# Kernel tuning notes

Hardware: AMD Instinct MI355X
Metric: run time of the kernel (lower is better)

The kernel has to match this reference:

```python
import jax, jax.numpy as jnp
import numpy as np

N = 50000      # nodes
E = 600000     # edges
C = 128        # input/output channels
H = 128        # hidden channels
EA = 8         # edge_attr_dim


def _lin_init(key, fan_in, fan_out):
    kw, kb = jax.random.split(key)
    w = jax.random.normal(kw, (fan_in, fan_out), dtype=jnp.float32) / np.sqrt(fan_in)
    b = jax.random.normal(kb, (fan_out,), dtype=jnp.float32) * 0.01
    return w, b


def setup_inputs() -> dict:
    key = jax.random.key(0)
    ks = jax.random.split(key, 8)
    x = jax.random.normal(ks[0], (N, C), dtype=jnp.float32)
    coord = jax.random.normal(ks[1], (N, 3), dtype=jnp.float32)
    edge_index = jax.random.randint(ks[2], (2, E), 0, N, dtype=jnp.int64)
    edge_attr = jax.random.normal(ks[3], (E, EA), dtype=jnp.float32)
    # edge_mlp: Linear(2C+1+EA -> H), ReLU, Linear(H -> H), ReLU
    w_e1, b_e1 = _lin_init(ks[4], 2 * C + 1 + EA, H)
    w_e2, b_e2 = _lin_init(ks[5], H, H)
    # node_mlp: Linear(H + C -> H), ReLU, Linear(H -> C)
    w_n1, b_n1 = _lin_init(ks[6], H + C, H)
    w_n2, b_n2 = _lin_init(ks[7], H, C)
    return {"x": x, "coord": coord, "edge_index": edge_index, "edge_attr": edge_attr,
            "w_e1": w_e1, "b_e1": b_e1, "w_e2": w_e2, "b_e2": b_e2,
            "w_n1": w_n1, "b_n1": b_n1, "w_n2": w_n2, "b_n2": b_n2}


def reference(x, coord, edge_index, edge_attr,
              w_e1, b_e1, w_e2, b_e2, w_n1, b_n1, w_n2, b_n2):
    row, col = edge_index[0], edge_index[1]
    # coord2radial: per-edge squared distance (coord_diff normalization unused
    # downstream since equivariant=False -> coord branch not taken)
    coord_diff = coord[row] - coord[col]                 # [E, 3]
    radial = jnp.sum(coord_diff * coord_diff, axis=1, keepdims=True)  # [E, 1]
    # edge_model: concat(source, target, radial, edge_attr) -> MLP
    e_in = jnp.concatenate([x[row], x[col], radial, edge_attr], axis=1)  # [E, 2C+1+EA]
    h = jax.nn.relu(e_in @ w_e1 + b_e1)
    edge_feat = jax.nn.relu(h @ w_e2 + b_e2)             # [E, H]
    # node_model: unsorted_segment_sum over row, concat with x, node MLP
    agg = jax.ops.segment_sum(edge_feat, row, num_segments=x.shape[0])  # [N, H]
    n_in = jnp.concatenate([x, agg], axis=1)             # [N, C+H]
    out = jax.nn.relu(n_in @ w_n1 + b_n1) @ w_n2 + b_n2  # [N, C]
    return out
```

## Files before the change

kernel.cpp:

```cpp
#include <hip/hip_runtime.h>

#define CH  128
#define HID 128
#define EAD 8

__device__ __forceinline__ void load8(const float* __restrict__ p, float* r) {
    float4 v0 = *(const float4*)p;
    float4 v1 = *(const float4*)(p + 4);
    r[0]=v0.x; r[1]=v0.y; r[2]=v0.z; r[3]=v0.w;
    r[4]=v1.x; r[5]=v1.y; r[6]=v1.z; r[7]=v1.w;
}
__device__ __forceinline__ void store8(float* p, const float* v) {
    *(float4*)p       = make_float4(v[0], v[1], v[2], v[3]);
    *(float4*)(p + 4) = make_float4(v[4], v[5], v[6], v[7]);
}
__device__ __forceinline__ void zero88(float a[8][8]) {
#pragma unroll
    for (int i = 0; i < 8; i++)
#pragma unroll
        for (int j = 0; j < 8; j++) a[i][j] = 0.f;
}

template <int K>
__device__ __forceinline__ void gemm_tile8(const float* sA, int strideA,
                                           const float* __restrict__ B, int ldb,
                                           int tr8, int jb, float acc[8][8]) {
#pragma unroll 2
    for (int k = 0; k < K; k += 4) {
        float av[8][4];
#pragma unroll
        for (int i = 0; i < 8; i++) {
            float4 t = *(const float4*)(sA + (tr8 + 8 * i) * strideA + k);
            av[i][0] = t.x; av[i][1] = t.y; av[i][2] = t.z; av[i][3] = t.w;
        }
#pragma unroll
        for (int kk = 0; kk < 4; kk++) {
            float b8[8];
            load8(B + (size_t)(k + kk) * ldb + jb, b8);
#pragma unroll
            for (int i = 0; i < 8; i++)
#pragma unroll
                for (int j = 0; j < 8; j++)
                    acc[i][j] = fmaf(av[i][kk], b8[j], acc[i][j]);
        }
    }
}

__global__ __launch_bounds__(128, 2)
void precompute_kernel(const float* __restrict__ x, const float* __restrict__ w1,
                       const float* __restrict__ b1, float* __restrict__ tbl, int N) {
    __shared__ float sX[64 * 132];
    const int tid = threadIdx.x;
    const int n0  = blockIdx.x * 64;
    {
        const int n = tid >> 1, q = tid & 1;
        int gn = n0 + n; if (gn >= N) gn = N - 1;
        const float4* src = (const float4*)(x + (size_t)gn * CH + q * 64);
        float4* dst = (float4*)(sX + n * 132 + q * 64);
#pragma unroll
        for (int u = 0; u < 16; u++) dst[u] = src[u];
    }
    __syncthreads();
    const int tr8 = tid & 7, jb = (tid >> 3) * 8;
    float acc[8][8];

    zero88(acc);
    gemm_tile8<128>(sX, 132, w1, HID, tr8, jb, acc);
    float bb[8]; load8(b1 + jb, bb);
#pragma unroll
    for (int i = 0; i < 8; i++) {
        const int gn = n0 + tr8 + 8 * i;
        if (gn < N) {
            float v[8];
#pragma unroll
            for (int j = 0; j < 8; j++) v[j] = acc[i][j] + bb[j];
            store8(tbl + (size_t)gn * 256 + jb, v);
        }
    }

    zero88(acc);
    gemm_tile8<128>(sX, 132, w1 + CH * HID, HID, tr8, jb, acc);
#pragma unroll
    for (int i = 0; i < 8; i++) {
        const int gn = n0 + tr8 + 8 * i;
        if (gn < N) store8(tbl + (size_t)gn * 256 + 128 + jb, acc[i]);
    }
}

__global__ void hist_kernel(const int* __restrict__ ei, int* __restrict__ deg, int E) {
    const int e = blockIdx.x * blockDim.x + threadIdx.x;
    if (e < E) atomicAdd(&deg[ei[e]], 1);
}

__global__ void scan_kernel(const int* __restrict__ deg, int* __restrict__ row_ptr,
                            int* __restrict__ cursor, int N) {
    __shared__ int part[1024];
    const int tid = threadIdx.x;
    const int chunk = (N + 1023) / 1024;
    const int lo = tid * chunk;
    const int hi = (lo + chunk < N) ? lo + chunk : N;
    int s = 0;
    for (int i = lo; i < hi; i++) s += deg[i];
    part[tid] = s;
    __syncthreads();
    for (int off = 1; off < 1024; off <<= 1) {
        int v = (tid >= off) ? part[tid - off] : 0;
        __syncthreads();
        part[tid] += v;
        __syncthreads();
    }
    int run = (tid == 0) ? 0 : part[tid - 1];
    for (int i = lo; i < hi; i++) {
        row_ptr[i] = run; cursor[i] = run;
        run += deg[i];
    }
    if (tid == 1023) row_ptr[N] = run;
}

__global__ void scatter_kernel(const int* __restrict__ ei, int* cursor,
                               int* __restrict__ perm, int E) {
    const int e = blockIdx.x * blockDim.x + threadIdx.x;
    if (e < E) {
        const int p = atomicAdd(&cursor[ei[e]], 1);
        perm[p] = e;
    }
}

__global__ __launch_bounds__(128, 2)
void edge_kernel_sorted(const float* __restrict__ tbl, const float* __restrict__ coord,
                        const int* __restrict__ ei, const float* __restrict__ ea,
                        const float* __restrict__ w1, const float* __restrict__ w2,
                        const float* __restrict__ b2, const int* __restrict__ perm,
                        const int* __restrict__ row_ptr, float* agg, int E) {
    __shared__ float sH[64 * 132];
    __shared__ float sW[9 * 128];
    __shared__ int   sRow[64];
    const int tid = threadIdx.x;

    const int nwg = gridDim.x;
    const int qq = nwg >> 3, rr = nwg & 7;
    const int xcd = blockIdx.x & 7, idx = blockIdx.x >> 3;
    const int wg  = (xcd < rr) ? (xcd * (qq + 1) + idx)
                               : (rr * (qq + 1) + (xcd - rr) * qq + idx);
    const int e0  = wg * 64;

    for (int i = tid; i < 9 * 128; i += 128) sW[i] = w1[256 * HID + i];
    __syncthreads();

    {
        const int s = tid >> 1, q = tid & 1;
        const int pe = perm[e0 + s];
        const int r = ei[pe];
        const int c = ei[E + pe];
        if (q == 0) sRow[s] = r;
        const float dx = coord[3 * r + 0] - coord[3 * c + 0];
        const float dy = coord[3 * r + 1] - coord[3 * c + 1];
        const float dz = coord[3 * r + 2] - coord[3 * c + 2];
        const float radial = fmaf(dx, dx, fmaf(dy, dy, dz * dz));
        float eav[8];
        load8(ea + (size_t)pe * EAD, eav);
        const float* tr = tbl + (size_t)r * 256 + q * 64;
        const float* tc = tbl + (size_t)c * 256 + 128 + q * 64;
        float* dst = sH + s * 132 + q * 64;
#pragma unroll
        for (int u = 0; u < 8; u++) {
            float hr[8], hc[8], wr[8], v[8];
            load8(tr + u * 8, hr);
            load8(tc + u * 8, hc);
            load8(sW + q * 64 + u * 8, wr);
#pragma unroll
            for (int j = 0; j < 8; j++) v[j] = hr[j] + hc[j] + radial * wr[j];
#pragma unroll
            for (int m = 0; m < 8; m++) {
                float we[8];
                load8(sW + (1 + m) * 128 + q * 64 + u * 8, we);
#pragma unroll
                for (int j = 0; j < 8; j++) v[j] = fmaf(eav[m], we[j], v[j]);
            }
#pragma unroll
            for (int j = 0; j < 8; j++) v[j] = fmaxf(v[j], 0.f);
            store8(dst + u * 8, v);
        }
    }
    __syncthreads();

    const int tr8 = tid & 7, jb = (tid >> 3) * 8;
    float acc[8][8];
    zero88(acc);
    gemm_tile8<128>(sH, 132, w2, HID, tr8, jb, acc);
    float bb[8]; load8(b2 + jb, bb);
    __syncthreads();

#pragma unroll
    for (int i = 0; i < 8; i++) {
        float v[8];
#pragma unroll
        for (int j = 0; j < 8; j++) v[j] = fmaxf(acc[i][j] + bb[j], 0.f);
        store8(sH + (tr8 + 8 * i) * 132 + jb, v);
    }
    __syncthreads();

#pragma unroll
    for (int base = 0; base < 64; base += 32) {
        const int s = base + (tid >> 2), q4 = tid & 3;
        const int r = sRow[s];
        const bool head = (s == 0) || (sRow[s - 1] != r);
        if (head) {
            float sum[32];
            const float* src = sH + s * 132 + q4 * 32;
#pragma unroll
            for (int j = 0; j < 32; j += 4) {
                float4 t = *(const float4*)(src + j);
                sum[j] = t.x; sum[j+1] = t.y; sum[j+2] = t.z; sum[j+3] = t.w;
            }
            int L = 1;
            while (s + L < 64 && sRow[s + L] == r) {
                const float* p = sH + (s + L) * 132 + q4 * 32;
#pragma unroll
                for (int j = 0; j < 32; j += 4) {
                    float4 t = *(const float4*)(p + j);
                    sum[j] += t.x; sum[j+1] += t.y; sum[j+2] += t.z; sum[j+3] += t.w;
                }
                L++;
            }
            float* dst = agg + (size_t)r * HID + q4 * 32;
            const bool interior = (row_ptr[r] >= e0) && (row_ptr[r + 1] <= e0 + 64);
            if (interior) {
#pragma unroll
                for (int j = 0; j < 32; j += 4)
                    *(float4*)(dst + j) = make_float4(sum[j], sum[j+1], sum[j+2], sum[j+3]);
            } else {
#pragma unroll
                for (int j = 0; j < 32; j++) atomicAdd(dst + j, sum[j]);
            }
        }
    }
}

__global__ __launch_bounds__(128, 2)
void node_kernel(const float* __restrict__ x, const float* agg,
                 const float* __restrict__ w1, const float* __restrict__ b1,
                 const float* __restrict__ w2, const float* __restrict__ b2,
                 float* out, int N) {
    __shared__ float sA[64 * 260];
    const int tid = threadIdx.x;
    const int n0  = blockIdx.x * 64;
    {
        const int n = tid >> 1, q = tid & 1;
        int gn = n0 + n; if (gn >= N) gn = N - 1;
        const float4* src = q ? (const float4*)(agg + (size_t)gn * HID)
                              : (const float4*)(x   + (size_t)gn * CH);
        float4* dst = (float4*)(sA + n * 260 + q * CH);
#pragma unroll
        for (int u = 0; u < 32; u++) dst[u] = src[u];
    }
    __syncthreads();
    const int tr8 = tid & 7, jb = (tid >> 3) * 8;
    float acc[8][8];
    zero88(acc);
    gemm_tile8<256>(sA, 260, w1, HID, tr8, jb, acc);
    float bb[8]; load8(b1 + jb, bb);
    float h[8][8];
#pragma unroll
    for (int i = 0; i < 8; i++)
#pragma unroll
        for (int j = 0; j < 8; j++) h[i][j] = fmaxf(acc[i][j] + bb[j], 0.f);
    __syncthreads();
#pragma unroll
    for (int i = 0; i < 8; i++) store8(sA + (tr8 + 8 * i) * 260 + jb, h[i]);
    __syncthreads();
    zero88(acc);
    gemm_tile8<128>(sA, 260, w2, CH, tr8, jb, acc);
    float b2v[8]; load8(b2 + jb, b2v);
#pragma unroll
    for (int i = 0; i < 8; i++) {
        const int gn = n0 + tr8 + 8 * i;
        if (gn < N) {
            float v[8];
#pragma unroll
            for (int j = 0; j < 8; j++) v[j] = acc[i][j] + b2v[j];
            store8(out + (size_t)gn * CH + jb, v);
        }
    }
}

extern "C" void kernel_launch(void* const* d_in, const int* in_sizes, int n_in,
                              void* d_out, int out_size, void* d_ws, size_t ws_size,
                              hipStream_t stream) {
    const float* x     = (const float*)d_in[0];
    const float* coord = (const float*)d_in[1];
    const int*   ei    = (const int*)d_in[2];
    const float* ea    = (const float*)d_in[3];
    const float* w_e1  = (const float*)d_in[4];
    const float* b_e1  = (const float*)d_in[5];
    const float* w_e2  = (const float*)d_in[6];
    const float* b_e2  = (const float*)d_in[7];
    const float* w_n1  = (const float*)d_in[8];
    const float* b_n1  = (const float*)d_in[9];
    const float* w_n2  = (const float*)d_in[10];
    const float* b_n2  = (const float*)d_in[11];

    const int N = in_sizes[0] / CH;
    const int E = in_sizes[2] / 2;

    float* out = (float*)d_out;
    float* agg = out;

    char* w = (char*)d_ws;
    float* tbl   = (float*)w;  w += (size_t)N * 256 * sizeof(float);
    int* perm    = (int*)w;    w += (size_t)E * sizeof(int);
    int* deg     = (int*)w;    w += (size_t)N * sizeof(int);
    int* row_ptr = (int*)w;    w += (size_t)(N + 1) * sizeof(int);
    int* cursor  = (int*)w;

    hipMemsetAsync(agg, 0, (size_t)N * HID * sizeof(float), stream);
    hipMemsetAsync(deg, 0, (size_t)N * sizeof(int), stream);

    precompute_kernel<<<dim3((N + 63) / 64), dim3(128), 0, stream>>>(x, w_e1, b_e1, tbl, N);
    hist_kernel<<<dim3((E + 255) / 256), dim3(256), 0, stream>>>(ei, deg, E);
    scan_kernel<<<dim3(1), dim3(1024), 0, stream>>>(deg, row_ptr, cursor, N);
    scatter_kernel<<<dim3((E + 255) / 256), dim3(256), 0, stream>>>(ei, cursor, perm, E);
    edge_kernel_sorted<<<dim3(E / 64), dim3(128), 0, stream>>>(tbl, coord, ei, ea,
                                                               w_e1, w_e2, b_e2,
                                                               perm, row_ptr, agg, E);
    node_kernel<<<dim3((N + 63) / 64), dim3(128), 0, stream>>>(x, agg, w_n1, b_n1,
                                                               w_n2, b_n2, out, N);
}
```

Before: 749.6 us.

## Use bf16 MFMA for edge second-layer GEMM with bf16 shared staging

Replaces the scalar FP32 register-tiled GEMM for the second edge MLP layer with bf16 MFMA 16x16x32 instructions. The hidden activations are staged in shared memory as bf16, and a new small kernel pre-transposes and converts w_e2 to bf16. This moves the per-edge 128x128 matmul onto the matrix cores and halves the LDS footprint, at the cost of bf16 rounding in both the hidden activations and the stored edge features before aggregation.

```diff
diff --git a/kernel.cpp b/kernel.cpp
--- a/kernel.cpp
+++ b/kernel.cpp
@@ -3,6 +3,9 @@
 #define CH  128
 #define HID 128
 #define EAD 8
+
+typedef __attribute__((ext_vector_type(8))) short short8v;
+typedef __attribute__((ext_vector_type(4))) float floatx4;
 
 __device__ __forceinline__ void load8(const float* __restrict__ p, float* r) {
     float4 v0 = *(const float4*)p;
@@ -19,6 +22,14 @@
     for (int i = 0; i < 8; i++)
 #pragma unroll
         for (int j = 0; j < 8; j++) a[i][j] = 0.f;
+}
+__device__ __forceinline__ unsigned short f2bf(float f) {
+    union { float f; unsigned u; } v; v.f = f;
+    return (unsigned short)((v.u + 0x7FFFu + ((v.u >> 16) & 1u)) >> 16);
+}
+__device__ __forceinline__ float bf2f(unsigned short h) {
+    union { unsigned u; float f; } v; v.u = ((unsigned)h) << 16;
+    return v.f;
 }
 
 template <int K>
@@ -126,13 +137,20 @@
     }
 }
 
+__global__ void prep_w2t(const float* __restrict__ w2, unsigned short* __restrict__ w2t) {
+    const int idx = blockIdx.x * 256 + threadIdx.x;
+    const int n = idx >> 7, k = idx & 127;
+    w2t[idx] = f2bf(w2[k * HID + n]);
+}
+
 __global__ __launch_bounds__(128, 2)
 void edge_kernel_sorted(const float* __restrict__ tbl, const float* __restrict__ coord,
                         const int* __restrict__ ei, const float* __restrict__ ea,
-                        const float* __restrict__ w1, const float* __restrict__ w2,
+                        const float* __restrict__ w1,
+                        const unsigned short* __restrict__ w2t,
                         const float* __restrict__ b2, const int* __restrict__ perm,
                         const int* __restrict__ row_ptr, float* agg, int E) {
-    __shared__ float sH[64 * 132];
+    __shared__ __align__(16) unsigned short sHu[64 * 136];
     __shared__ float sW[9 * 128];
     __shared__ int   sRow[64];
     const int tid = threadIdx.x;
@@ -161,7 +179,7 @@
         load8(ea + (size_t)pe * EAD, eav);
         const float* tr = tbl + (size_t)r * 256 + q * 64;
         const float* tc = tbl + (size_t)c * 256 + 128 + q * 64;
-        float* dst = sH + s * 132 + q * 64;
+        unsigned short* dst = sHu + s * 136 + q * 64;
 #pragma unroll
         for (int u = 0; u < 8; u++) {
             float hr[8], hc[8], wr[8], v[8];
@@ -177,27 +195,60 @@
 #pragma unroll
                 for (int j = 0; j < 8; j++) v[j] = fmaf(eav[m], we[j], v[j]);
             }
-#pragma unroll
-            for (int j = 0; j < 8; j++) v[j] = fmaxf(v[j], 0.f);
-            store8(dst + u * 8, v);
-        }
-    }
-    __syncthreads();
-
-    const int tr8 = tid & 7, jb = (tid >> 3) * 8;
-    float acc[8][8];
-    zero88(acc);
-    gemm_tile8<128>(sH, 132, w2, HID, tr8, jb, acc);
-    float bb[8]; load8(b2 + jb, bb);
-    __syncthreads();
-
-#pragma unroll
-    for (int i = 0; i < 8; i++) {
-        float v[8];
-#pragma unroll
-        for (int j = 0; j < 8; j++) v[j] = fmaxf(acc[i][j] + bb[j], 0.f);
-        store8(sH + (tr8 + 8 * i) * 132 + jb, v);
-    }
+            short8v t;
+#pragma unroll
+            for (int j = 0; j < 8; j++) t[j] = (short)f2bf(fmaxf(v[j], 0.f));
+            *(short8v*)(dst + u * 8) = t;
+        }
+    }
+    __syncthreads();
+
+    const int lane = tid & 63;
+    const int wcol = (tid >> 6) * 64;
+    const int lr = lane & 15;
+    const int lg = lane >> 4;
+    floatx4 acc[4][4];
+#pragma unroll
+    for (int mt = 0; mt < 4; mt++)
+#pragma unroll
+        for (int ct = 0; ct < 4; ct++)
+#pragma unroll
+            for (int j = 0; j < 4; j++) acc[mt][ct][j] = 0.f;
+
+#pragma unroll
+    for (int kc = 0; kc < 4; kc++) {
+        short8v afr[4];
+#pragma unroll
+        for (int mt = 0; mt < 4; mt++)
+            afr[mt] = *(const short8v*)(sHu + (mt * 16 + lr) * 136 + kc * 32 + lg * 8);
+        short8v bfr[4];
+#pragma unroll
+        for (int ct = 0; ct < 4; ct++)
+            bfr[ct] = *(const short8v*)(w2t + (size_t)(wcol + ct * 16 + lr) * HID
+                                            + kc * 32 + lg * 8);
+#pragma unroll
+        for (int mt = 0; mt < 4; mt++)
+#pragma unroll
+            for (int ct = 0; ct < 4; ct++)
+                acc[mt][ct] = __builtin_amdgcn_mfma_f32_16x16x32_bf16(
+                                  afr[mt], bfr[ct], acc[mt][ct], 0, 0, 0);
+    }
+
+    float b2v[4];
+#pragma unroll
+    for (int ct = 0; ct < 4; ct++) b2v[ct] = b2[wcol + ct * 16 + lr];
+    __syncthreads();
+
+#pragma unroll
+    for (int mt = 0; mt < 4; mt++)
+#pragma unroll
+        for (int ct = 0; ct < 4; ct++)
+#pragma unroll
+            for (int r_ = 0; r_ < 4; r_++) {
+                const int row = mt * 16 + lg * 4 + r_;
+                const int col = wcol + ct * 16 + lr;
+                sHu[row * 136 + col] = f2bf(fmaxf(acc[mt][ct][r_] + b2v[ct], 0.f));
+            }
     __syncthreads();
 
 #pragma unroll
@@ -207,19 +258,25 @@
         const bool head = (s == 0) || (sRow[s - 1] != r);
         if (head) {
             float sum[32];
-            const float* src = sH + s * 132 + q4 * 32;
-#pragma unroll
-            for (int j = 0; j < 32; j += 4) {
-                float4 t = *(const float4*)(src + j);
-                sum[j] = t.x; sum[j+1] = t.y; sum[j+2] = t.z; sum[j+3] = t.w;
+            {
+                const short8v* sp = (const short8v*)(sHu + s * 136 + q4 * 32);
+#pragma unroll
+                for (int v8 = 0; v8 < 4; v8++) {
+                    short8v t = sp[v8];
+#pragma unroll
+                    for (int j = 0; j < 8; j++)
+                        sum[v8 * 8 + j] = bf2f((unsigned short)t[j]);
+                }
             }
             int L = 1;
             while (s + L < 64 && sRow[s + L] == r) {
-                const float* p = sH + (s + L) * 132 + q4 * 32;
-#pragma unroll
-                for (int j = 0; j < 32; j += 4) {
-                    float4 t = *(const float4*)(p + j);
-                    sum[j] += t.x; sum[j+1] += t.y; sum[j+2] += t.z; sum[j+3] += t.w;
+                const short8v* sp = (const short8v*)(sHu + (s + L) * 136 + q4 * 32);
+#pragma unroll
+                for (int v8 = 0; v8 < 4; v8++) {
+                    short8v t = sp[v8];
+#pragma unroll
+                    for (int j = 0; j < 8; j++)
+                        sum[v8 * 8 + j] += bf2f((unsigned short)t[j]);
                 }
                 L++;
             }
@@ -307,21 +364,23 @@
     float* agg = out;
 
     char* w = (char*)d_ws;
-    float* tbl   = (float*)w;  w += (size_t)N * 256 * sizeof(float);
-    int* perm    = (int*)w;    w += (size_t)E * sizeof(int);
-    int* deg     = (int*)w;    w += (size_t)N * sizeof(int);
-    int* row_ptr = (int*)w;    w += (size_t)(N + 1) * sizeof(int);
+    float* tbl   = (float*)w;          w += (size_t)N * 256 * sizeof(float);
+    int* perm    = (int*)w;            w += (size_t)E * sizeof(int);
+    unsigned short* w2t = (unsigned short*)w;  w += (size_t)HID * HID * 2;
+    int* deg     = (int*)w;            w += (size_t)N * sizeof(int);
+    int* row_ptr = (int*)w;            w += (size_t)(N + 1) * sizeof(int);
     int* cursor  = (int*)w;
 
     hipMemsetAsync(agg, 0, (size_t)N * HID * sizeof(float), stream);
     hipMemsetAsync(deg, 0, (size_t)N * sizeof(int), stream);
 
     precompute_kernel<<<dim3((N + 63) / 64), dim3(128), 0, stream>>>(x, w_e1, b_e1, tbl, N);
+    prep_w2t<<<dim3(HID * HID / 256), dim3(256), 0, stream>>>(w_e2, w2t);
     hist_kernel<<<dim3((E + 255) / 256), dim3(256), 0, stream>>>(ei, deg, E);
     scan_kernel<<<dim3(1), dim3(1024), 0, stream>>>(deg, row_ptr, cursor, N);
     scatter_kernel<<<dim3((E + 255) / 256), dim3(256), 0, stream>>>(ei, cursor, perm, E);
     edge_kernel_sorted<<<dim3(E / 64), dim3(128), 0, stream>>>(tbl, coord, ei, ea,
-                                                               w_e1, w_e2, b_e2,
+                                                               w_e1, w2t, b_e2,
                                                                perm, row_ptr, agg, E);
     node_kernel<<<dim3((N + 63) / 64), dim3(128), 0, stream>>>(x, agg, w_n1, b_n1,
                                                                w_n2, b_n2, out, N);
```

New measurement: 666.2 us. 1.13x faster.
